# Optimization experiments

Hardware: AMD Instinct MI355X
Metric: run time of the kernel (lower is better)

## Reference

```python
import jax, jax.numpy as jnp
import numpy as np
from jax import lax

POOL = 4  # hp['gcn_pool_size']


def sparsemax(z):
    # sparsemax along last axis (Martins & Astudillo 2016), matches tfa.activations.sparsemax
    n = z.shape[-1]
    z_sorted = jnp.flip(jnp.sort(z, axis=-1), axis=-1)          # descending
    k = jnp.arange(1, n + 1, dtype=z.dtype)
    zcum = jnp.cumsum(z_sorted, axis=-1)
    support = (1.0 + k * z_sorted) > zcum                        # [.., n] bool
    k_sel = jnp.sum(support, axis=-1, keepdims=True)             # int, >= 1
    tau = (jnp.take_along_axis(zcum, k_sel - 1, axis=-1) - 1.0) / k_sel.astype(z.dtype)
    return jnp.maximum(z - tau, 0.0)


def gcn_layer(x, W):
    # x: [B, T, E]
    T = x.shape[1]
    # einsum('Bte,bte->tBb') then mean over t == contract over t,e and divide by T
    adj = jnp.einsum('Bte,bte->Bb', x, x) / T                    # [B, B]
    adj = sparsemax(adj)                                         # row-wise sparsemax
    m = adj[:, :, None, None] * x[None]                          # [B, b, T, E] outer product
    # MaxPool2D((POOL,1), stride 1, 'same') on [batch=B, H=b, W=T, C=E]: pool over neighbor axis b
    m = lax.reduce_window(m, -jnp.inf, lax.max,
                          (1, POOL, 1, 1), (1, 1, 1, 1), 'SAME')
    agg = jnp.sum(m, axis=1)                                     # [B, T, E]
    return jax.nn.relu(agg @ W)                                  # [B, T, rel_dim]


def setup_inputs() -> dict:
    key = jax.random.key(0)
    k0, k1, k2, k3 = jax.random.split(key, 4)
    B, T, E = 64, 256, 64
    rel_dim, n_stack = 4, 8
    x = jax.random.normal(k0, (B, T, E), dtype=jnp.float32)
    W0 = jax.random.normal(k1, (E, rel_dim), dtype=jnp.float32) * 0.1
    W1 = jax.random.normal(k2, (rel_dim, rel_dim), dtype=jnp.float32) * 0.1
    Wp = jax.random.normal(k3, (rel_dim, n_stack), dtype=jnp.float32) * 0.1
    return {"x": x, "W0": W0, "W1": W1, "Wp": Wp}


def reference(x, W0, W1, Wp):
    x = gcn_layer(x, W0)           # layer 0: E -> rel_dim
    x = gcn_layer(x, W1)           # layer 1: rel_dim -> rel_dim
    pooled = jnp.mean(x, axis=1)   # [B, rel_dim], mean over T
    return jax.nn.softmax(pooled @ Wp, axis=-1)  # [B, n_stack]
```

## Files before the change

### kernel.cpp

```cpp
#include <hip/hip_runtime.h>
#include <math.h>

__device__ __forceinline__ float4 f4max(float4 a, float4 b) {
    return make_float4(fmaxf(a.x, b.x), fmaxf(a.y, b.y), fmaxf(a.z, b.z), fmaxf(a.w, b.w));
}
__device__ __forceinline__ float4 f4scale(float s, float4 v) {
    return make_float4(s * v.x, s * v.y, s * v.z, s * v.w);
}
__device__ __forceinline__ float4 f4add(float4 a, float4 b) {
    return make_float4(a.x + b.x, a.y + b.y, a.z + b.z, a.w + b.w);
}
__device__ __forceinline__ float4 f4fma(float a, float4 b, float4 c) {
    return make_float4(fmaf(a, b.x, c.x), fmaf(a, b.y, c.y), fmaf(a, b.z, c.z), fmaf(a, b.w, c.w));
}
__device__ __forceinline__ float4 f4fma4(float4 a, float4 b, float4 c) {
    return make_float4(fmaf(a.x, b.x, c.x), fmaf(a.y, b.y, c.y),
                       fmaf(a.z, b.z, c.z), fmaf(a.w, b.w, c.w));
}

__device__ __forceinline__ void store_f4_llc(float* p, float4 v) {
    __hip_atomic_store(p + 0, v.x, __ATOMIC_RELAXED, __HIP_MEMORY_SCOPE_AGENT);
    __hip_atomic_store(p + 1, v.y, __ATOMIC_RELAXED, __HIP_MEMORY_SCOPE_AGENT);
    __hip_atomic_store(p + 2, v.z, __ATOMIC_RELAXED, __HIP_MEMORY_SCOPE_AGENT);
    __hip_atomic_store(p + 3, v.w, __ATOMIC_RELAXED, __HIP_MEMORY_SCOPE_AGENT);
}

__device__ __forceinline__ float wave_sparsemax(float z, int lane) {
    float v = z;
    for (int k = 2; k <= 64; k <<= 1) {
        bool desc = (lane & k) == 0;
        for (int j = k >> 1; j > 0; j >>= 1) {
            float other = __shfl_xor(v, j, 64);
            bool lower = (lane & j) == 0;
            float mn = fminf(v, other), mx = fmaxf(v, other);
            v = (desc ^ lower) ? mn : mx;
        }
    }
    float c = v;
    for (int d = 1; d < 64; d <<= 1) {
        float n = __shfl_up(c, d, 64);
        if (lane >= d) c += n;
    }
    bool sup = (1.0f + (float)(lane + 1) * v) > c;
    int ksel = __popcll(__ballot(sup));
    float zk = __shfl(c, ksel - 1, 64);
    float tau = (zk - 1.0f) / (float)ksel;
    return fmaxf(z - tau, 0.f);
}

__device__ unsigned g_grp[16 * 64];
__device__ unsigned g_glb;
__device__ unsigned g_gen1;
__device__ unsigned g_gen2;

__device__ __forceinline__ void sync_point(int bx, unsigned snap, unsigned* genp,
                                           bool wait) {
    __syncthreads();
    if (threadIdx.x == 0) {
        unsigned a = __hip_atomic_fetch_add(&g_grp[(bx & 15) << 6], 1u,
                                            __ATOMIC_RELAXED, __HIP_MEMORY_SCOPE_AGENT);
        if ((a & 15u) == 15u) {
            unsigned ga = __hip_atomic_fetch_add(&g_glb, 1u, __ATOMIC_RELAXED,
                                                 __HIP_MEMORY_SCOPE_AGENT);
            if ((ga & 15u) == 15u)
                __hip_atomic_fetch_add(genp, 1u, __ATOMIC_RELAXED,
                                       __HIP_MEMORY_SCOPE_AGENT);
        }
        if (wait) {
            while (__hip_atomic_load(genp, __ATOMIC_RELAXED,
                                     __HIP_MEMORY_SCOPE_AGENT) == snap)
                __builtin_amdgcn_s_sleep(1);
            __builtin_amdgcn_fence(__ATOMIC_ACQUIRE, "agent");
        }
    }
    if (wait) __syncthreads();
}

__global__ __launch_bounds__(256)
void fused_gcn(const float* __restrict__ x, const float* __restrict__ W0,
               const float* __restrict__ W1, const float* __restrict__ Wp,
               float* __restrict__ P, float* __restrict__ h0,
               float* __restrict__ out) {
    __shared__ float xsT[64][68];
    __shared__ float pst[4][4][64];
    __shared__ float psm_s[4][4][64];
    __shared__ __align__(16) float row[4 * 260];
    __shared__ float part[256];
    __shared__ float psmD[64];
    __shared__ float red[16];

    int tid = threadIdx.x;
    int bx = blockIdx.x;
    int lane = tid & 63;

    unsigned snap1 = 0, snap2 = 0;
    if (tid == 0) {
        snap1 = __hip_atomic_load(&g_gen1, __ATOMIC_RELAXED, __HIP_MEMORY_SCOPE_AGENT);
        snap2 = __hip_atomic_load(&g_gen2, __ATOMIC_RELAXED, __HIP_MEMORY_SCOPE_AGENT);
    }

    {
        int k0 = bx * 64;
#pragma unroll
        for (int it = 0; it < 4; ++it) {
            int f = it * 256 + tid;
            int i = f >> 4, k4 = (f & 15) * 4;
            float4 v = *(const float4*)(x + (size_t)i * 16384 + k0 + k4);
            xsT[k4 + 0][i] = v.x; xsT[k4 + 1][i] = v.y;
            xsT[k4 + 2][i] = v.z; xsT[k4 + 3][i] = v.w;
        }
        __syncthreads();
        int ti = (tid >> 4) * 4, tj = (tid & 15) * 4;
        float4 a0 = make_float4(0, 0, 0, 0), a1 = a0, a2 = a0, a3 = a0;
#pragma unroll 8
        for (int k = 0; k < 64; ++k) {
            float4 a = *(const float4*)&xsT[k][ti];
            float4 b = *(const float4*)&xsT[k][tj];
            a0 = f4fma(a.x, b, a0); a1 = f4fma(a.y, b, a1);
            a2 = f4fma(a.z, b, a2); a3 = f4fma(a.w, b, a3);
        }
        float* basep = P + ((size_t)bx << 12);
        store_f4_llc(basep + (ti + 0) * 64 + tj, a0);
        store_f4_llc(basep + (ti + 1) * 64 + tj, a1);
        store_f4_llc(basep + (ti + 2) * 64 + tj, a2);
        store_f4_llc(basep + (ti + 3) * 64 + tj, a3);
    }
    sync_point(bx, snap1, &g_gen1, true);

    {
        int w4 = tid >> 6;
        int Bc = (bx & 3) * 16;
        int rr = (tid & 63) >> 4;
        int c4 = (tid & 15) * 4;
        const float* pb = P + (size_t)(Bc + (w4 << 2) + rr) * 64 + c4;
        float4 g[4];
#pragma unroll
        for (int gg = 0; gg < 4; ++gg) {
            float4 s = make_float4(0, 0, 0, 0);
#pragma unroll 8
            for (int c = gg * 64; c < gg * 64 + 64; ++c)
                s = f4add(s, *(const float4*)(pb + ((size_t)c << 12)));
            g[gg] = s;
        }
        float4 s = f4add(f4add(f4add(g[0], g[1]), g[2]), g[3]);
        *(float4*)&pst[w4][rr][c4] = s;
        __syncthreads();
#pragma unroll
        for (int h = 0; h < 4; ++h) {
            float z = pst[w4][h][lane] * (1.0f / 256.0f);
            psm_s[w4][h][lane] = wave_sparsemax(z, lane);
        }
        __syncthreads();
    }

    {
        int t0 = (bx >> 2) * 4;
        int Bc = (bx & 3) * 16;
        int w = __builtin_amdgcn_readfirstlane(tid >> 6);
        int t = lane >> 4, eq = lane & 15;
        float4 w0r0 = *(const float4*)(W0 + (eq * 4 + 0) * 4);
        float4 w0r1 = *(const float4*)(W0 + (eq * 4 + 1) * 4);
        float4 w0r2 = *(const float4*)(W0 + (eq * 4 + 2) * 4);
        float4 w0r3 = *(const float4*)(W0 + (eq * 4 + 3) * 4);
        const float4* xg = (const float4*)(x + ((size_t)(t0 + t) * 64) + eq * 4);
        float4 qm1[4], qb[4], vt[4], acc[4];
        float4 xA = xg[0];
        float4 xB = xg[4096];
#pragma unroll
        for (int h = 0; h < 4; ++h) {
            float4 v = f4scale(psm_s[w][h][0], xA);
            vt[h] = f4scale(psm_s[w][h][1], xB);
            qm1[h] = v;
            qb[h] = f4max(v, vt[h]);
            acc[h] = make_float4(0, 0, 0, 0);
        }
#pragma unroll 4
        for (int bl = 0; bl < 62; ++bl) {
            float4 xn = xg[(size_t)(bl + 2) * 4096];
#pragma unroll
            for (int h = 0; h < 4; ++h) {
                float4 vn = f4scale(psm_s[w][h][bl + 2], xn);
                float4 q1 = f4max(vt[h], vn);
                acc[h] = f4add(acc[h], f4max(qm1[h], q1));
                qm1[h] = qb[h]; qb[h] = q1; vt[h] = vn;
            }
        }
#pragma unroll
        for (int h = 0; h < 4; ++h) {
            acc[h] = f4add(acc[h], f4max(qm1[h], vt[h]));
            acc[h] = f4add(acc[h], qb[h]);
            float4 a = acc[h];
            float4 hh = f4fma(a.x, w0r0, f4fma(a.y, w0r1,
                       f4fma(a.z, w0r2, f4scale(a.w, w0r3))));
            for (int m = 1; m <= 8; m <<= 1) {
                hh.x += __shfl_xor(hh.x, m, 64);
                hh.y += __shfl_xor(hh.y, m, 64);
                hh.z += __shfl_xor(hh.z, m, 64);
                hh.w += __shfl_xor(hh.w, m, 64);
            }
            if (eq == 0) {
                int B = Bc + 4 * w + h;
                float4 r = make_float4(fmaxf(hh.x, 0.f), fmaxf(hh.y, 0.f),
                                       fmaxf(hh.z, 0.f), fmaxf(hh.w, 0.f));
                store_f4_llc(h0 + (size_t)(B * 256 + t0 + t) * 4, r);
            }
        }
    }
    sync_point(bx, snap2, &g_gen2, bx < 64);

    if (bx < 64) {
        int bid = bx;
        {
            int q = tid >> 6, s2 = (tid & 63) * 4;
            *(float4*)(row + q * 260 + s2) = *(const float4*)(h0 + (size_t)bid * 1024 + tid * 4);
        }
        __syncthreads();
        {
            int j = tid >> 2, q = tid & 3;
            const float4* hj = (const float4*)(h0 + (size_t)j * 1024 + q * 256);
            const float4* ri = (const float4*)(row + q * 260);
            float4 s4 = make_float4(0, 0, 0, 0);
#pragma unroll 8
            for (int kk = 0; kk < 64; ++kk) s4 = f4fma4(ri[kk], hj[kk], s4);
            part[tid] = s4.x + s4.y + s4.z + s4.w;
        }
        __syncthreads();
        if (tid < 64) {
            float z = (part[lane * 4] + part[lane * 4 + 1] + part[lane * 4 + 2]
                       + part[lane * 4 + 3]) * (1.0f / 256.0f);
            psmD[lane] = wave_sparsemax(z, lane);
        }
        __syncthreads();
        int w = __builtin_amdgcn_readfirstlane(tid >> 6);
        int rc = lane & 3;
        float psum = 0.f;
#pragma unroll
        for (int gg = 0; gg < 4; ++gg) {
            int tbase = w * 64 + gg * 16;
            const float* xb = h0 + (size_t)tbase * 4 + lane;
            float v0 = psmD[0] * xb[0];
            float v1 = psmD[1] * xb[1024];
            float qm1s = v0, qbs = fmaxf(v0, v1), vts = v1, accs = 0.f;
#pragma unroll 8
            for (int bl = 0; bl < 62; ++bl) {
                float vn = psmD[bl + 2] * xb[(size_t)(bl + 2) * 1024];
                float q1 = fmaxf(vts, vn);
                accs += fmaxf(qm1s, q1);
                qm1s = qbs; qbs = q1; vts = vn;
            }
            accs += fmaxf(qm1s, vts);
            accs += qbs;
            int base = lane & ~3;
            float b0 = __shfl(accs, base + 0, 64);
            float b1 = __shfl(accs, base + 1, 64);
            float b2 = __shfl(accs, base + 2, 64);
            float b3 = __shfl(accs, base + 3, 64);
            float h = b0 * W1[rc] + b1 * W1[4 + rc] + b2 * W1[8 + rc] + b3 * W1[12 + rc];
            psum += fmaxf(h, 0.f);
        }
        for (int m = 4; m <= 32; m <<= 1) psum += __shfl_xor(psum, m, 64);
        if (lane < 4) red[w * 4 + lane] = psum;
        __syncthreads();
        if (tid < 64) {
            float pooled = 0.f;
            if (lane < 4)
                pooled = (red[lane] + red[4 + lane] + red[8 + lane] + red[12 + lane])
                         * (1.0f / 256.0f);
            float q0 = __shfl(pooled, 0, 64), q1 = __shfl(pooled, 1, 64);
            float q2 = __shfl(pooled, 2, 64), q3 = __shfl(pooled, 3, 64);
            float logit = -INFINITY;
            if (lane < 8)
                logit = q0 * Wp[lane] + q1 * Wp[8 + lane]
                      + q2 * Wp[16 + lane] + q3 * Wp[24 + lane];
            float mx = logit;
            for (int m = 4; m >= 1; m >>= 1) mx = fmaxf(mx, __shfl_xor(mx, m, 8));
            float e = (lane < 8) ? __expf(logit - mx) : 0.f;
            float s = e;
            for (int m = 4; m >= 1; m >>= 1) s += __shfl_xor(s, m, 8);
            if (lane < 8) out[bid * 8 + lane] = e / s;
        }
    }
}

extern "C" void kernel_launch(void* const* d_in, const int* in_sizes, int n_in,
                              void* d_out, int out_size, void* d_ws, size_t ws_size,
                              hipStream_t stream) {
    const float* x  = (const float*)d_in[0];
    const float* W0 = (const float*)d_in[1];
    const float* W1 = (const float*)d_in[2];
    const float* Wp = (const float*)d_in[3];
    float* out = (float*)d_out;

    char* ws = (char*)d_ws;
    float* P  = (float*)ws;
    float* h0 = (float*)(ws + (4u << 20));

    fused_gcn<<<256, 256, 0, stream>>>(x, W0, W1, Wp, P, h0, out);
}
```

Baseline: 129.8 us.

## Remap layer-0 work so each block handles 4 rows over 16 timesteps

Changes the per-block decomposition of layer 0. Each block now owns 4 adjacency rows and 16 timesteps instead of 16 rows and 4 timesteps. The P reduction is split across four sub-groups of 64 partials plus a small shared-memory combine, so each block reduces only 4 rows instead of 16, cutting redundant global reads of the partial Gram matrices. The four waves now share one sparsemax row set. In exchange, x is reloaded by 16 blocks per timestep group instead of 4 per row group.

```diff
diff --git a/kernel.cpp b/kernel.cpp
--- a/kernel.cpp
+++ b/kernel.cpp
@@ -82,8 +82,8 @@
                float* __restrict__ P, float* __restrict__ h0,
                float* __restrict__ out) {
     __shared__ float xsT[64][68];
-    __shared__ float pst[4][4][64];
-    __shared__ float psm_s[4][4][64];
+    __shared__ float pstg[4][4][64];
+    __shared__ float psm_s[4][64];
     __shared__ __align__(16) float row[4 * 260];
     __shared__ float part[256];
     __shared__ float psmD[64];
@@ -129,47 +129,44 @@
 
     {
         int w4 = tid >> 6;
-        int Bc = (bx & 3) * 16;
-        int rr = (tid & 63) >> 4;
-        int c4 = (tid & 15) * 4;
-        const float* pb = P + (size_t)(Bc + (w4 << 2) + rr) * 64 + c4;
-        float4 g[4];
-#pragma unroll
-        for (int gg = 0; gg < 4; ++gg) {
-            float4 s = make_float4(0, 0, 0, 0);
-#pragma unroll 8
-            for (int c = gg * 64; c < gg * 64 + 64; ++c)
-                s = f4add(s, *(const float4*)(pb + ((size_t)c << 12)));
-            g[gg] = s;
-        }
-        float4 s = f4add(f4add(f4add(g[0], g[1]), g[2]), g[3]);
-        *(float4*)&pst[w4][rr][c4] = s;
-        __syncthreads();
-#pragma unroll
-        for (int h = 0; h < 4; ++h) {
-            float z = pst[w4][h][lane] * (1.0f / 256.0f);
-            psm_s[w4][h][lane] = wave_sparsemax(z, lane);
+        int Bc = (bx & 15) * 4;
+        int rowi = Bc + w4;
+        int sub = (tid & 63) >> 4;
+        int c16 = tid & 15;
+        const float* pb = P + (size_t)rowi * 64 + c16 * 4;
+        float4 g = make_float4(0, 0, 0, 0);
+        int cbase = sub * 64;
+#pragma unroll 8
+        for (int i = 0; i < 64; ++i)
+            g = f4add(g, *(const float4*)(pb + ((size_t)(cbase + i) << 12)));
+        *(float4*)&pstg[w4][sub][c16 * 4] = g;
+        __syncthreads();
+        {
+            float z = (((pstg[w4][0][lane] + pstg[w4][1][lane])
+                        + pstg[w4][2][lane]) + pstg[w4][3][lane]) * (1.0f / 256.0f);
+            psm_s[w4][lane] = wave_sparsemax(z, lane);
         }
         __syncthreads();
     }
 
     {
-        int t0 = (bx >> 2) * 4;
-        int Bc = (bx & 3) * 16;
+        int t0 = (bx >> 4) * 16;
+        int Bc = (bx & 15) * 4;
         int w = __builtin_amdgcn_readfirstlane(tid >> 6);
-        int t = lane >> 4, eq = lane & 15;
+        int tq = lane >> 4, eq = lane & 15;
+        int t = t0 + (w << 2) + tq;
         float4 w0r0 = *(const float4*)(W0 + (eq * 4 + 0) * 4);
         float4 w0r1 = *(const float4*)(W0 + (eq * 4 + 1) * 4);
         float4 w0r2 = *(const float4*)(W0 + (eq * 4 + 2) * 4);
         float4 w0r3 = *(const float4*)(W0 + (eq * 4 + 3) * 4);
-        const float4* xg = (const float4*)(x + ((size_t)(t0 + t) * 64) + eq * 4);
+        const float4* xg = (const float4*)(x + ((size_t)t * 64) + eq * 4);
         float4 qm1[4], qb[4], vt[4], acc[4];
         float4 xA = xg[0];
         float4 xB = xg[4096];
 #pragma unroll
         for (int h = 0; h < 4; ++h) {
-            float4 v = f4scale(psm_s[w][h][0], xA);
-            vt[h] = f4scale(psm_s[w][h][1], xB);
+            float4 v = f4scale(psm_s[h][0], xA);
+            vt[h] = f4scale(psm_s[h][1], xB);
             qm1[h] = v;
             qb[h] = f4max(v, vt[h]);
             acc[h] = make_float4(0, 0, 0, 0);
@@ -179,7 +176,7 @@
             float4 xn = xg[(size_t)(bl + 2) * 4096];
 #pragma unroll
             for (int h = 0; h < 4; ++h) {
-                float4 vn = f4scale(psm_s[w][h][bl + 2], xn);
+                float4 vn = f4scale(psm_s[h][bl + 2], xn);
                 float4 q1 = f4max(vt[h], vn);
                 acc[h] = f4add(acc[h], f4max(qm1[h], q1));
                 qm1[h] = qb[h]; qb[h] = q1; vt[h] = vn;
@@ -199,10 +196,10 @@
                 hh.w += __shfl_xor(hh.w, m, 64);
             }
             if (eq == 0) {
-                int B = Bc + 4 * w + h;
+                int B = Bc + h;
                 float4 r = make_float4(fmaxf(hh.x, 0.f), fmaxf(hh.y, 0.f),
                                        fmaxf(hh.z, 0.f), fmaxf(hh.w, 0.f));
-                store_f4_llc(h0 + (size_t)(B * 256 + t0 + t) * 4, r);
+                store_f4_llc(h0 + (size_t)(B * 256 + t) * 4, r);
             }
         }
     }
```

Measured after the change: 116.5 us. -10.3%, faster.
